# Kernel optimization log

Measured on AMD Instinct MI355X. Metric: run time of the kernel, lower is better.

Reference implementation:

```python
import jax, jax.numpy as jnp
import numpy as np

DIM = 512
HEADS = 8
DIM_HEAD = 64
INNER = HEADS * DIM_HEAD          # 512
CPB_DIM = DIM // 2                # 256 (ContinuousPositionBias hidden dim)
FF_INNER = int(DIM * 4 * 2 / 3)   # 1365 (GEGLU inner dim)
B, C, F, H, W = 2, 512, 8, 32, 32
SCALE = DIM_HEAD ** -0.5


def setup_inputs() -> dict:
    key = jax.random.key(0)
    ks = jax.random.split(key, 24)
    def rnd(k, shape, s=0.02):
        return jax.random.normal(k, shape, jnp.float32) * s
    return {
        "x": jax.random.normal(ks[0], (B, C, F, W, W), jnp.float32)[:, :, :, :H, :],
        # spatial attention
        "sa_gamma": jnp.ones((DIM,), jnp.float32),
        "sa_wq": rnd(ks[1], (DIM, INNER)),
        "sa_wkv": rnd(ks[2], (DIM, 2 * INNER)),
        "sa_wo": rnd(ks[3], (INNER, DIM)),
        # temporal attention
        "ta_gamma": jnp.ones((DIM,), jnp.float32),
        "ta_wq": rnd(ks[4], (DIM, INNER)),
        "ta_wkv": rnd(ks[5], (DIM, 2 * INNER)),
        "ta_wo": rnd(ks[6], (INNER, DIM)),
        # spatial ContinuousPositionBias MLP (num_dims=2, layers=2)
        "sp_w1": rnd(ks[7], (2, CPB_DIM), 0.1), "sp_b1": jnp.zeros((CPB_DIM,), jnp.float32),
        "sp_w2": rnd(ks[8], (CPB_DIM, CPB_DIM), 0.05), "sp_b2": jnp.zeros((CPB_DIM,), jnp.float32),
        "sp_w3": rnd(ks[9], (CPB_DIM, HEADS), 0.05), "sp_b3": jnp.zeros((HEADS,), jnp.float32),
        # temporal ContinuousPositionBias MLP (num_dims=1)
        "tp_w1": rnd(ks[10], (1, CPB_DIM), 0.1), "tp_b1": jnp.zeros((CPB_DIM,), jnp.float32),
        "tp_w2": rnd(ks[11], (CPB_DIM, CPB_DIM), 0.05), "tp_b2": jnp.zeros((CPB_DIM,), jnp.float32),
        "tp_w3": rnd(ks[12], (CPB_DIM, HEADS), 0.05), "tp_b3": jnp.zeros((HEADS,), jnp.float32),
        # FeedForward: Conv3d 1x1 (no bias) -> GEGLU -> RMSNorm -> Conv3d 1x1
        "ff_win": rnd(ks[13], (DIM, 2 * FF_INNER)),
        "ff_gamma": jnp.ones((FF_INNER,), jnp.float32),
        "ff_wout": rnd(ks[14], (FF_INNER, DIM)),
    }


def _rms_last(x, g):
    # torch: F.normalize(x, dim=-1) * sqrt(C) * gamma
    nrm = jnp.sqrt(jnp.sum(x * x, axis=-1, keepdims=True))
    return x / jnp.maximum(nrm, 1e-12) * jnp.sqrt(jnp.float32(x.shape[-1])) * g


def _mlp_bias(rel, w1, b1, w2, b2, w3, b3):
    h = jax.nn.silu(rel @ w1 + b1)
    h = jax.nn.silu(h @ w2 + b2)
    return h @ w3 + b3  # [R, heads]


def _cpb_2d(h, w, params):
    ry = jnp.arange(-(h - 1), h, dtype=jnp.float32)
    rx = jnp.arange(-(w - 1), w, dtype=jnp.float32)
    gy, gx = jnp.meshgrid(ry, rx, indexing='ij')
    rel = jnp.stack([gy, gx], -1).reshape(-1, 2)          # [(2h-1)(2w-1), 2]
    tab = _mlp_bias(rel, *params)                          # [R, heads]
    py, px = jnp.meshgrid(jnp.arange(h), jnp.arange(w), indexing='ij')
    pos = jnp.stack([py.reshape(-1), px.reshape(-1)], -1)  # [n, 2]
    d = pos[:, None, :] - pos[None, :, :]                  # [n, n, 2]
    idx = (d[..., 0] + h - 1) * (2 * w - 1) + (d[..., 1] + w - 1)
    return jnp.transpose(tab[idx], (2, 0, 1))              # [heads, n, n]


def _cpb_1d(f, params):
    rel = jnp.arange(-(f - 1), f, dtype=jnp.float32)[:, None]
    tab = _mlp_bias(rel, *params)                          # [2f-1, heads]
    p = jnp.arange(f)
    idx = p[:, None] - p[None, :] + f - 1
    return jnp.transpose(tab[idx], (2, 0, 1))              # [heads, f, f]


def _attn(x, gamma, wq, wkv, wo, bias):
    # x: [b, n, c]; manual softmax(QK^T*scale + bias)V (flash disabled by pos_bias)
    xn = _rms_last(x, gamma)
    q = xn @ wq
    k, v = jnp.split(xn @ wkv, 2, axis=-1)
    b, n, _ = q.shape
    rs = lambda t: t.reshape(b, n, HEADS, DIM_HEAD).transpose(0, 2, 1, 3)
    q, k, v = rs(q), rs(k), rs(v)
    s = jnp.einsum('bhid,bhjd->bhij', q, k) * SCALE + bias[None]
    a = jax.nn.softmax(s, axis=-1)
    o = jnp.einsum('bhij,bhjd->bhid', a, v)
    o = o.transpose(0, 2, 1, 3).reshape(b, n, INNER)
    return o @ wo


def _ff(x, win, gamma, wout):
    # x: [b, f, h, w, c] channel-last; Conv3d 1x1 == channel einsum
    hdn = jnp.einsum('bfhwc,co->bfhwo', x, win)
    a, gate = jnp.split(hdn, 2, axis=-1)
    y = a * jax.nn.gelu(gate, approximate=False)           # GEGLU (torch exact gelu)
    # shift_token: chunk channels, shift second half by +1 frame
    c1 = (FF_INNER + 1) // 2
    t1, t2 = y[..., :c1], y[..., c1:]
    t2 = jnp.pad(t2, ((0, 0), (1, 0), (0, 0), (0, 0), (0, 0)))[:, :-1]
    y = jnp.concatenate([t1, t2], axis=-1)
    yn = _rms_last(y, gamma)                               # RMSNorm over channels
    return jnp.einsum('bfhwi,ic->bfhwc', yn, wout)


def reference(x, sa_gamma, sa_wq, sa_wkv, sa_wo, ta_gamma, ta_wq, ta_wkv, ta_wo,
              sp_w1, sp_b1, sp_w2, sp_b2, sp_w3, sp_b3,
              tp_w1, tp_b1, tp_w2, tp_b2, tp_w3, tp_b3,
              ff_win, ff_gamma, ff_wout):
    b, c, f, h, w = x.shape
    xl = jnp.transpose(x, (0, 2, 3, 4, 1))                 # b f h w c
    # spatial attention over (h w) tokens, batched over (b f)
    xs = xl.reshape(b * f, h * w, c)
    sp_bias = _cpb_2d(h, w, (sp_w1, sp_b1, sp_w2, sp_b2, sp_w3, sp_b3))
    xs = _attn(xs, sa_gamma, sa_wq, sa_wkv, sa_wo, sp_bias) + xs
    xv = xs.reshape(b, f, h, w, c)
    # temporal attention over f tokens, batched over (b h w)
    xt = jnp.transpose(xv, (0, 2, 3, 1, 4)).reshape(b * h * w, f, c)
    tp_bias = _cpb_1d(f, (tp_w1, tp_b1, tp_w2, tp_b2, tp_w3, tp_b3))
    xt = _attn(xt, ta_gamma, ta_wq, ta_wkv, ta_wo, tp_bias) + xt
    xv = jnp.transpose(xt.reshape(b, h, w, f, c), (0, 3, 1, 2, 4))
    # GEGLU feedforward with token shift
    xv = _ff(xv, ff_win, ff_gamma, ff_wout) + xv
    return jnp.transpose(xv, (0, 4, 1, 2, 3))              # b c f h w
```

## Files before the change

kernel.cpp:

```cpp
#include <hip/hip_runtime.h>
#include <cstdint>
#include <cstddef>

typedef __bf16 bf16_t;
typedef __bf16 bf16x8 __attribute__((ext_vector_type(8)));
typedef __bf16 bf16x4 __attribute__((ext_vector_type(4)));
typedef float floatx4 __attribute__((ext_vector_type(4)));

__device__ __forceinline__ float wred_sum(float v) {
#pragma unroll
  for (int off = 32; off > 0; off >>= 1) v += __shfl_xor(v, off);
  return v;
}
__device__ __forceinline__ void async16(const void* g, void* l) {
  __builtin_amdgcn_global_load_lds((const __attribute__((address_space(1))) void*)g,
                                   (__attribute__((address_space(3))) void*)l, 16, 0, 0);
}

template <int MODE>
__global__ __launch_bounds__(256) void st_gemm(
    const bf16_t* __restrict__ A, const bf16_t* __restrict__ B, void* Cp, void* Cp2,
    const float* Res, int M, int N, int K, int lda, int ldb, int ldc, int nb1,
    long long sa1, long long sa2, long long sb1, long long sb2,
    long long sc1, long long sc2) {
  __shared__ bf16_t sA[128 * 32];
  __shared__ bf16_t sB[128 * 32];
  const int z = blockIdx.z;
  const int z1 = z % nb1, z2 = z / nb1;
  A += z1 * sa1 + z2 * sa2;
  B += z1 * sb1 + z2 * sb2;
  const long long coff = z1 * sc1 + z2 * sc2;
  const int tid = threadIdx.x;
  const int bm = blockIdx.x, bn = blockIdx.y;
  const int lane = tid & 63;
  const int wave = tid >> 6;
  const int wm = (wave >> 1) * 64, wn = (wave & 1) * 64;
  const int rowf = lane & 15, qc = lane >> 4;
  const int fco = (qc ^ ((rowf >> 1) & 3)) * 8;

  const bf16_t* aSrc[2];
  const bf16_t* bSrc[2];
  char* aDst[2];
  char* bDst[2];
#pragma unroll
  for (int it = 0; it < 2; ++it) {
    int slot = it * 256 + tid;
    int mi = slot >> 2, kc = slot & 3;
    int cs = kc ^ ((mi >> 1) & 3);
    int ar = bm * 128 + mi; if (ar > M - 1) ar = M - 1;
    int br = bn * 128 + mi; if (br > N - 1) br = N - 1;
    aSrc[it] = A + (size_t)ar * lda + cs * 8;
    bSrc[it] = B + (size_t)br * ldb + cs * 8;
    aDst[it] = (char*)sA + slot * 16;
    bDst[it] = (char*)sB + slot * 16;
  }

  floatx4 acc[4][4];
#pragma unroll
  for (int i = 0; i < 4; ++i)
#pragma unroll
    for (int j = 0; j < 4; ++j) acc[i][j] = floatx4{0.f, 0.f, 0.f, 0.f};

  for (int kt = 0; kt < K; kt += 32) {
#pragma unroll
    for (int it = 0; it < 2; ++it) {
      async16(aSrc[it] + kt, aDst[it]);
      async16(bSrc[it] + kt, bDst[it]);
    }
    __syncthreads();
    bf16x8 af[4], bv[4];
#pragma unroll
    for (int i = 0; i < 4; ++i) {
      af[i] = *(const bf16x8*)(sA + (wm + i * 16 + rowf) * 32 + fco);
      bv[i] = *(const bf16x8*)(sB + (wn + i * 16 + rowf) * 32 + fco);
    }
#pragma unroll
    for (int i = 0; i < 4; ++i)
#pragma unroll
      for (int j = 0; j < 4; ++j)
        acc[i][j] = __builtin_amdgcn_mfma_f32_16x16x32_bf16(af[i], bv[j], acc[i][j], 0, 0, 0);
    __syncthreads();
  }

  const int cl = lane & 15;
  const int rowBase = bm * 128 + wm + (lane >> 4) * 4;
  if (MODE == 5) {
    bf16_t* yb = (bf16_t*)Cp;
    const int cg0 = ((bn * 128 + wn) >> 5) * 16;
#pragma unroll
    for (int i = 0; i < 4; ++i) {
#pragma unroll
      for (int p = 0; p < 2; ++p) {
        int c = cg0 + p * 16 + cl;
        if (c >= 1365) continue;
#pragma unroll
        for (int r = 0; r < 4; ++r) {
          int row = rowBase + i * 16 + r;
          if (row >= M) continue;
          float a = acc[i][2 * p][r];
          float gt = acc[i][2 * p + 1][r];
          float zz = gt * (0.7978845608f + 0.03567740814f * gt * gt);
          float u = __builtin_exp2f(-2.8853900817779268f * zz);
          float y = a * gt / (1.f + u);
          yb[(size_t)row * ldc + c] = (bf16_t)y;
        }
      }
    }
    return;
  }
  const int colBase = bn * 128 + wn + cl;
#pragma unroll
  for (int i = 0; i < 4; ++i) {
#pragma unroll
    for (int j = 0; j < 4; ++j) {
      int col = colBase + j * 16;
      if (col >= N) continue;
#pragma unroll
      for (int r = 0; r < 4; ++r) {
        int row = rowBase + i * 16 + r;
        if (row >= M) continue;
        long long inidx = coff + (long long)row * ldc + col;
        float v = acc[i][j][r];
        if (MODE >= 2) v += Res[inidx];
        if (MODE == 0) { ((float*)Cp)[inidx] = v; }
        else if (MODE == 1) { ((bf16_t*)Cp)[inidx] = (bf16_t)v; }
        else if (MODE == 2) { ((float*)Cp)[inidx] = v; }
        else if (MODE == 3) {
          int orow = (row & ~8191) | ((row & 1023) << 3) | ((row >> 10) & 7);
          ((float*)Cp)[coff + (long long)orow * ldc + col] = v;
        } else if (MODE == 4) {
          int orow = (row & ~8191) | ((row & 7) << 10) | ((row >> 3) & 1023);
          long long oidx = coff + (long long)orow * ldc + col;
          ((float*)Cp)[oidx] = v;
          ((bf16_t*)Cp2)[oidx] = (bf16_t)v;
        }
      }
    }
  }
}

__global__ __launch_bounds__(256) void st_transpose2d(
    const float* __restrict__ in, float* __restrict__ out, int R, int Cc,
    long long inb, long long outb) {
  __shared__ float tile[32][33];
  const int ct = blockIdx.x, rt = blockIdx.y, b = blockIdx.z;
  in += (long long)b * inb;
  out += (long long)b * outb;
  const int tx = threadIdx.x & 31, ty = threadIdx.x >> 5;
#pragma unroll
  for (int k = 0; k < 4; ++k) {
    int r = rt * 32 + ty + k * 8;
    int c = ct * 32 + tx;
    tile[ty + k * 8][tx] = in[(size_t)r * Cc + c];
  }
  __syncthreads();
#pragma unroll
  for (int k = 0; k < 4; ++k) {
    int c = ct * 32 + ty + k * 8;
    int r = rt * 32 + tx;
    out[(size_t)c * R + r] = tile[tx][ty + k * 8];
  }
}

__global__ void st_wtrans(const float* __restrict__ src, bf16_t* __restrict__ dst,
                          int K, int Kpad, int N, int srcld, int coloff, long total) {
  long idx = (long)blockIdx.x * 256 + threadIdx.x;
  if (idx >= total) return;
  int kp = (int)(idx % Kpad);
  int n = (int)(idx / Kpad);
  float v = (kp < K) ? src[(size_t)kp * srcld + coloff + n] : 0.f;
  dst[idx] = (bf16_t)v;
}

__global__ void st_wtrans_geglu(const float* __restrict__ src, bf16_t* __restrict__ dst,
                                long total) {
  long idx = (long)blockIdx.x * 256 + threadIdx.x;
  if (idx >= total) return;
  int kp = (int)(idx & 511);
  int n = (int)(idx >> 9);
  int c = ((n >> 5) << 4) + (n & 15);
  float v = 0.f;
  if (c < 1365) {
    int srccol = c + (((n >> 4) & 1) ? 1365 : 0);
    v = src[(size_t)kp * 2730 + srccol];
  }
  dst[idx] = (bf16_t)v;
}

__global__ __launch_bounds__(256) void st_cpb(
    const float* __restrict__ w1, const float* __restrict__ b1,
    const float* __restrict__ w2, const float* __restrict__ b2,
    const float* __restrict__ w3, const float* __restrict__ b3,
    float* __restrict__ tab2d, float* __restrict__ tab1d, int two_d) {
  const int pos = blockIdx.x, t = threadIdx.x;
  float r0, r1 = 0.f;
  if (two_d) { r0 = (float)(pos / 63 - 31); r1 = (float)(pos % 63 - 31); }
  else { r0 = (float)(pos - 7); }
  __shared__ float sh[256];
  float h = r0 * w1[t] + (two_d ? r1 * w1[256 + t] : 0.f) + b1[t];
  h = h / (1.f + expf(-h));
  sh[t] = h;
  __syncthreads();
  float h2 = b2[t];
  for (int j = 0; j < 256; ++j) h2 += sh[j] * w2[j * 256 + t];
  h2 = h2 / (1.f + expf(-h2));
  __syncthreads();
  sh[t] = h2;
  __syncthreads();
  if (t < 8) {
    float o = b3[t];
    for (int j = 0; j < 256; ++j) o += sh[j] * w3[j * 8 + t];
    if (two_d) tab2d[t * 4000 + pos] = o * 8.0f;
    else tab1d[t * 15 + pos] = o;
  }
}

__global__ __launch_bounds__(256) void st_rmsnorm(const float* __restrict__ x,
                                                  const float* __restrict__ gamma,
                                                  bf16_t* __restrict__ y) {
  const int token = blockIdx.x * 4 + (threadIdx.x >> 6);
  const int lane = threadIdx.x & 63;
  const float* xr = x + (size_t)token * 512;
  float v[8];
  float ss = 0.f;
#pragma unroll
  for (int k = 0; k < 8; ++k) { v[k] = xr[k * 64 + lane]; ss += v[k] * v[k]; }
  ss = wred_sum(ss);
  const float r = 22.627416998f / fmaxf(sqrtf(ss), 1e-12f);
  bf16_t* yr = y + (size_t)token * 512;
#pragma unroll
  for (int k = 0; k < 8; ++k) yr[k * 64 + lane] = (bf16_t)(v[k] * r * gamma[k * 64 + lane]);
}

__global__ __launch_bounds__(256) void st_vtrans(const bf16_t* __restrict__ qkv,
                                                 bf16_t* __restrict__ vT) {
  __shared__ float tile[32][33];
  const int jt = blockIdx.x, dt = blockIdx.y, z = blockIdx.z;
  const int bf = z >> 3, h = z & 7;
  const int tx = threadIdx.x & 31, ty = threadIdx.x >> 5;
#pragma unroll
  for (int k = 0; k < 4; ++k) {
    int j = jt * 32 + ty + k * 8;
    int d = dt * 32 + tx;
    tile[ty + k * 8][tx] = (float)qkv[((size_t)(bf * 1024 + j)) * 1536 + 1024 + h * 64 + d];
  }
  __syncthreads();
#pragma unroll
  for (int k = 0; k < 4; ++k) {
    int d = dt * 32 + ty + k * 8;
    int j = jt * 32 + tx;
    vT[((size_t)z * 64 + d) * 1024 + j] = (bf16_t)tile[tx][ty + k * 8];
  }
}

__global__ __launch_bounds__(256, 4) void st_flash(
    const bf16_t* __restrict__ qkv, const bf16_t* __restrict__ vT,
    const float* __restrict__ tab2f, bf16_t* __restrict__ ob) {
  __shared__ __align__(16) bf16_t ldsK[2][32 * 64];
  __shared__ __align__(16) bf16_t ldsV[2][64 * 32];
  __shared__ __align__(16) bf16_t ldsP[4 * 32 * 32];
  __shared__ __align__(16) float ldsT[2208];
  const int qtile = blockIdx.x;
  const int z = blockIdx.y;
  const int bf = z >> 3, h = z & 7;
  const int tid = threadIdx.x;
  const int lane = tid & 63, wave = tid >> 6;
  const int cl = lane & 15, g = lane >> 4;
  const size_t qkvBase = (size_t)bf * 1024 * 1536 + h * 64;
  const int eoff = (qtile * 252) & ~3;
  const bf16_t* Kp = qkv + qkvBase + 512;
  const bf16_t* Vp = vT + (size_t)z * 65536;

#pragma unroll
  for (int it = 0; it < 3; ++it) {
    int s = it * 256 + tid;
    if (s < 552) async16(tab2f + h * 4000 + eoff + s * 4, (char*)ldsT + s * 16);
  }
  {
    int row = tid >> 3, c = tid & 7, cs = c ^ (row & 7);
    async16(Kp + (size_t)row * 1536 + cs * 8, (char*)ldsK[0] + tid * 16);
    int rv = tid >> 2, cv = tid & 3, csv = cv ^ (rv & 3);
    async16(Vp + (size_t)rv * 1024 + csv * 8, (char*)ldsV[0] + tid * 16);
  }
  bf16x8 aq[2][2];
#pragma unroll
  for (int it = 0; it < 2; ++it)
#pragma unroll
    for (int ks = 0; ks < 2; ++ks) {
      int row = qtile * 128 + wave * 32 + it * 16 + cl;
      aq[it][ks] = *(const bf16x8*)(qkv + qkvBase + (size_t)row * 1536 + (ks * 4 + g) * 8);
    }
  __syncthreads();

  int fiB[2];
#pragma unroll
  for (int it = 0; it < 2; ++it) {
    int i = qtile * 128 + wave * 32 + it * 16 + cl;
    fiB[it] = (i >> 5) * 63 + (i & 31) + 1984 - eoff;
  }
  float lsum[2] = {0.f, 0.f};
  floatx4 oacc[4][2];
#pragma unroll
  for (int dt = 0; dt < 4; ++dt)
#pragma unroll
    for (int it = 0; it < 2; ++it) oacc[dt][it] = floatx4{0.f, 0.f, 0.f, 0.f};

  bf16_t* ldsPw = ldsP + wave * (32 * 32);
  const float SC = 0.18033688011112042f;

#pragma unroll 2
  for (int t = 0; t < 32; ++t) {
    const int p = t & 1;
    if (t < 31) {
      const int j1 = (t + 1) * 32;
      int row = tid >> 3, c = tid & 7, cs = c ^ (row & 7);
      async16(Kp + (size_t)(j1 + row) * 1536 + cs * 8, (char*)ldsK[p ^ 1] + tid * 16);
      int rv = tid >> 2, cv = tid & 3, csv = cv ^ (rv & 3);
      async16(Vp + (size_t)rv * 1024 + j1 + csv * 8, (char*)ldsV[p ^ 1] + tid * 16);
    }
    const int j0 = t * 32;
#pragma unroll
    for (int jt = 0; jt < 2; ++jt) {
      int jb = j0 + jt * 16 + g * 4;
      int fjb = (jb >> 5) * 63 + (jb & 31);
      floatx4 sj[2];
#pragma unroll
      for (int it = 0; it < 2; ++it) {
        int idx0 = fiB[it] - fjb;
        sj[it] = floatx4{ldsT[idx0], ldsT[idx0 - 1], ldsT[idx0 - 2], ldsT[idx0 - 3]};
      }
#pragma unroll
      for (int ks = 0; ks < 2; ++ks) {
        int row = jt * 16 + cl;
        bf16x8 kf = *(const bf16x8*)(ldsK[p] + row * 64 + (((ks * 4 + g) ^ (row & 7))) * 8);
#pragma unroll
        for (int it = 0; it < 2; ++it)
          sj[it] = __builtin_amdgcn_mfma_f32_16x16x32_bf16(kf, aq[it][ks], sj[it], 0, 0, 0);
      }
      int gg = jt * 2 + (g >> 1);
#pragma unroll
      for (int it = 0; it < 2; ++it) {
        float e0 = __builtin_exp2f(sj[it][0] * SC);
        float e1 = __builtin_exp2f(sj[it][1] * SC);
        float e2 = __builtin_exp2f(sj[it][2] * SC);
        float e3 = __builtin_exp2f(sj[it][3] * SC);
        lsum[it] += (e0 + e1) + (e2 + e3);
        bf16x4 pv = {(bf16_t)e0, (bf16_t)e1, (bf16_t)e2, (bf16_t)e3};
        *(bf16x4*)((char*)ldsPw + (it * 16 + cl) * 64 +
                   ((gg ^ (cl & 3)) * 16 + (g & 1) * 8)) = pv;
      }
    }
    {
      bf16x8 pB[2];
#pragma unroll
      for (int it = 0; it < 2; ++it)
        pB[it] = *(const bf16x8*)((char*)ldsPw + (it * 16 + cl) * 64 + ((g ^ (cl & 3)) * 16));
#pragma unroll
      for (int dt = 0; dt < 4; ++dt) {
        int row = dt * 16 + cl;
        bf16x8 vf = *(const bf16x8*)(ldsV[p] + row * 32 + ((g ^ (row & 3)) * 8));
#pragma unroll
        for (int it = 0; it < 2; ++it)
          oacc[dt][it] = __builtin_amdgcn_mfma_f32_16x16x32_bf16(vf, pB[it], oacc[dt][it], 0, 0, 0);
      }
    }
    __syncthreads();
  }
  float inv[2];
#pragma unroll
  for (int it = 0; it < 2; ++it) {
    float s = lsum[it];
    s += __shfl_xor(s, 16);
    s += __shfl_xor(s, 32);
    inv[it] = 1.f / s;
  }
#pragma unroll
  for (int it = 0; it < 2; ++it) {
    int i = qtile * 128 + wave * 32 + it * 16 + cl;
    size_t base = ((size_t)bf * 1024 + i) * 512 + h * 64 + g * 4;
#pragma unroll
    for (int dt = 0; dt < 4; ++dt) {
      bf16x4 ov = {(bf16_t)(oacc[dt][it][0] * inv[it]), (bf16_t)(oacc[dt][it][1] * inv[it]),
                   (bf16_t)(oacc[dt][it][2] * inv[it]), (bf16_t)(oacc[dt][it][3] * inv[it])};
      *(bf16x4*)(ob + base + dt * 16) = ov;
    }
  }
}

__global__ __launch_bounds__(256) void st_tattn2(const bf16_t* __restrict__ qkv,
                                                 const float* __restrict__ tabf,
                                                 bf16_t* __restrict__ o) {
  const int wg = blockIdx.x * 4 + (threadIdx.x >> 6);
  const int bhw = wg >> 3, head = wg & 7;
  const int lane = threadIdx.x & 63;
  const size_t base = (size_t)bhw * 8 * 1536 + head * 64 + lane;
  float q[8], k[8], v[8];
#pragma unroll
  for (int f = 0; f < 8; ++f) {
    q[f] = (float)qkv[base + (size_t)f * 1536];
    k[f] = (float)qkv[base + (size_t)f * 1536 + 512];
    v[f] = (float)qkv[base + (size_t)f * 1536 + 1024];
  }
  float p[64];
#pragma unroll
  for (int i = 0; i < 8; ++i)
#pragma unroll
    for (int j = 0; j < 8; ++j) p[i * 8 + j] = q[i] * k[j];
#pragma unroll
  for (int st = 32; st >= 1; st >>= 1) {
    const bool hi = (lane & st) != 0;
#pragma unroll
    for (int m = 0; m < st; ++m) {
      float give = hi ? p[m] : p[m + st];
      float keep = hi ? p[m + st] : p[m];
      p[m] = keep + __shfl_xor(give, st);
    }
  }
  const int i = lane >> 3, j = lane & 7;
  float e = __expf(p[0] * 0.125f + tabf[head * 15 + i - j + 7]);
  float sm = e;
  sm += __shfl_xor(sm, 1);
  sm += __shfl_xor(sm, 2);
  sm += __shfl_xor(sm, 4);
  const float prob = e / sm;
  float acc[8];
#pragma unroll
  for (int ii = 0; ii < 8; ++ii) acc[ii] = 0.f;
#pragma unroll
  for (int ii = 0; ii < 8; ++ii)
#pragma unroll
    for (int jj = 0; jj < 8; ++jj)
      acc[ii] += __shfl(prob, ii * 8 + jj) * v[jj];
#pragma unroll
  for (int ii = 0; ii < 8; ++ii)
    o[(size_t)(bhw * 8 + ii) * 512 + head * 64 + lane] = (bf16_t)acc[ii];
}

__global__ __launch_bounds__(256) void st_glu(const bf16_t* __restrict__ y,
                                              const float* __restrict__ gamma,
                                              bf16_t* __restrict__ yn) {
  const int t = blockIdx.x;
  const int tid = threadIdx.x;
  const int f = (t >> 10) & 7;
  float yv[6];
  float ss = 0.f;
#pragma unroll
  for (int kk = 0; kk < 6; ++kk) {
    int c = kk * 256 + tid;
    float v = 0.f;
    if (c < 1365) {
      long src = t;
      bool valid = true;
      if (c >= 683) { if (f == 0) valid = false; else src = t - 1024; }
      if (valid) v = (float)y[src * 1365 + c];
    }
    yv[kk] = v;
    ss += v * v;
  }
  __shared__ float red[4];
  ss = wred_sum(ss);
  if ((tid & 63) == 0) red[tid >> 6] = ss;
  __syncthreads();
  ss = red[0] + red[1] + red[2] + red[3];
  const float r = sqrtf(1365.f) / fmaxf(sqrtf(ss), 1e-12f);
#pragma unroll
  for (int kk = 0; kk < 6; ++kk) {
    int c = kk * 256 + tid;
    if (c < 1365) yn[(size_t)t * 1376 + c] = (bf16_t)(yv[kk] * r * gamma[c]);
  }
  if (tid < 11) yn[(size_t)t * 1376 + 1365 + tid] = (bf16_t)0.f;
}

extern "C" void kernel_launch(void* const* d_in, const int* in_sizes, int n_in,
                              void* d_out, int out_size, void* d_ws, size_t ws_size,
                              hipStream_t stream) {
  const float* x        = (const float*)d_in[0];
  const float* sa_gamma = (const float*)d_in[1];
  const float* sa_wq    = (const float*)d_in[2];
  const float* sa_wkv   = (const float*)d_in[3];
  const float* sa_wo    = (const float*)d_in[4];
  const float* ta_gamma = (const float*)d_in[5];
  const float* ta_wq    = (const float*)d_in[6];
  const float* ta_wkv   = (const float*)d_in[7];
  const float* ta_wo    = (const float*)d_in[8];
  const float* sp_w1 = (const float*)d_in[9];
  const float* sp_b1 = (const float*)d_in[10];
  const float* sp_w2 = (const float*)d_in[11];
  const float* sp_b2 = (const float*)d_in[12];
  const float* sp_w3 = (const float*)d_in[13];
  const float* sp_b3 = (const float*)d_in[14];
  const float* tp_w1 = (const float*)d_in[15];
  const float* tp_b1 = (const float*)d_in[16];
  const float* tp_w2 = (const float*)d_in[17];
  const float* tp_b2 = (const float*)d_in[18];
  const float* tp_w3 = (const float*)d_in[19];
  const float* tp_b3 = (const float*)d_in[20];
  const float* ff_win   = (const float*)d_in[21];
  const float* ff_gamma = (const float*)d_in[22];
  const float* ff_wout  = (const float*)d_in[23];
  float* outp = (float*)d_out;

  char* ws = (char*)d_ws;
  size_t off = 0;
  auto alloc = [&](size_t bytes) -> char* {
    char* p = ws + off;
    off += (bytes + 255) & ~(size_t)255;
    return p;
  };
  const long T = 16384;
  float*  xs  = (float*)alloc((size_t)T * 512 * 4);
  bf16_t* xn  = (bf16_t*)alloc((size_t)T * 512 * 2);
  char*   R2  = alloc((size_t)T * 1536 * 2);
  char*   R3  = alloc((size_t)T * 1536 * 2);
  char*   R4  = alloc((size_t)T * 1376 * 2);
  bf16_t* wqkvT_sa = (bf16_t*)alloc(1536ULL * 512 * 2);
  bf16_t* woT_sa   = (bf16_t*)alloc(512ULL * 512 * 2);
  bf16_t* wqkvT_ta = (bf16_t*)alloc(1536ULL * 512 * 2);
  bf16_t* woT_ta   = (bf16_t*)alloc(512ULL * 512 * 2);
  bf16_t* winT  = (bf16_t*)alloc(2752ULL * 512 * 2);
  bf16_t* woutT = (bf16_t*)alloc(512ULL * 1376 * 2);
  float*  tab2f = (float*)alloc(8 * 4000 * 4);
  float*  tabf  = (float*)alloc(8 * 15 * 4);

  bf16_t* qkv  = (bf16_t*)R2;
  bf16_t* ybuf = (bf16_t*)R2;
  bf16_t* vT   = (bf16_t*)R3;
  float*  xt   = (float*)R3;
  bf16_t* ob_s = xn;
  bf16_t* ob_t = (bf16_t*)R4;
  bf16_t* ynb  = (bf16_t*)R4;

  st_transpose2d<<<dim3(256, 16, 2), 256, 0, stream>>>(x, xs, 512, 8192,
                                                       (long long)512 * 8192, (long long)512 * 8192);
  auto wt = [&](const float* src, bf16_t* dst, int K, int Kpad, int N, int srcld, int coloff) {
    long tot = (long)N * Kpad;
    st_wtrans<<<dim3((tot + 255) / 256), 256, 0, stream>>>(src, dst, K, Kpad, N, srcld, coloff, tot);
  };
  wt(sa_wq, wqkvT_sa, 512, 512, 512, 512, 0);
  wt(sa_wkv, wqkvT_sa + 512 * 512, 512, 512, 1024, 1024, 0);
  wt(sa_wo, woT_sa, 512, 512, 512, 512, 0);
  wt(ta_wq, wqkvT_ta, 512, 512, 512, 512, 0);
  wt(ta_wkv, wqkvT_ta + 512 * 512, 512, 512, 1024, 1024, 0);
  wt(ta_wo, woT_ta, 512, 512, 512, 512, 0);
  st_wtrans_geglu<<<dim3((2752 * 512) / 256), 256, 0, stream>>>(ff_win, winT, 2752L * 512);
  wt(ff_wout, woutT, 1365, 1376, 512, 512, 0);
  st_cpb<<<dim3(3969), 256, 0, stream>>>(sp_w1, sp_b1, sp_w2, sp_b2, sp_w3, sp_b3, tab2f, tabf, 1);
  st_cpb<<<dim3(15), 256, 0, stream>>>(tp_w1, tp_b1, tp_w2, tp_b2, tp_w3, tp_b3, tab2f, tabf, 0);

  st_rmsnorm<<<dim3(4096), 256, 0, stream>>>(xs, sa_gamma, xn);
  st_gemm<1><<<dim3(128, 12, 1), 256, 0, stream>>>(
      xn, wqkvT_sa, (void*)qkv, nullptr, nullptr, 16384, 1536, 512, 512, 512, 1536, 1, 0, 0, 0, 0, 0, 0);
  st_vtrans<<<dim3(32, 2, 128), 256, 0, stream>>>(qkv, vT);
  st_flash<<<dim3(8, 128), 256, 0, stream>>>(qkv, vT, tab2f, ob_s);
  st_gemm<3><<<dim3(128, 4, 1), 256, 0, stream>>>(
      ob_s, woT_sa, (void*)xt, nullptr, xs, 16384, 512, 512, 512, 512, 512, 1, 0, 0, 0, 0, 0, 0);

  st_rmsnorm<<<dim3(4096), 256, 0, stream>>>(xt, ta_gamma, xn);
  st_gemm<1><<<dim3(128, 12, 1), 256, 0, stream>>>(
      xn, wqkvT_ta, (void*)qkv, nullptr, nullptr, 16384, 1536, 512, 512, 512, 1536, 1, 0, 0, 0, 0, 0, 0);
  st_tattn2<<<dim3(4096), 256, 0, stream>>>(qkv, tabf, ob_t);
  st_gemm<4><<<dim3(128, 4, 1), 256, 0, stream>>>(
      ob_t, woT_ta, (void*)xs, (void*)xn, xt, 16384, 512, 512, 512, 512, 512, 1, 0, 0, 0, 0, 0, 0);

  st_gemm<5><<<dim3(128, 22, 1), 256, 0, stream>>>(
      xn, winT, (void*)ybuf, nullptr, nullptr, 16384, 2752, 512, 512, 512, 1365, 1, 0, 0, 0, 0, 0, 0);
  st_glu<<<dim3(16384), 256, 0, stream>>>(ybuf, ff_gamma, ynb);
  st_gemm<2><<<dim3(128, 4, 1), 256, 0, stream>>>(
      ynb, woutT, (void*)xs, nullptr, xs, 16384, 512, 1376, 1376, 1376, 512, 1, 0, 0, 0, 0, 0, 0);

  st_transpose2d<<<dim3(16, 256, 2), 256, 0, stream>>>(xs, outp, 8192, 512,
                                                       (long long)8192 * 512, (long long)8192 * 512);
}
```

Baseline: 685.7 us.

## Add 256x256-tile triple-buffered GEMM for QKV and GEGLU projections

Adds a new 512-thread GEMM kernel with 256x256 output tiles, a three-stage async global-to-LDS buffer ring, split A/B prefetch interleaved with MFMA phases, s_setprio around the MFMA blocks, and a swizzled block order for L2 locality. It replaces the two QKV projections and the GEGLU input projection. The GEGLU weight is padded to 2816 columns so the N dimension divides the larger tile. The intent is more reuse per tile and hiding load latency behind compute. The cost is more LDS and registers per block and fewer blocks in flight. The old kernel's batching arguments and MODE 5 path are removed.

```diff
diff --git a/kernel.cpp b/kernel.cpp
--- a/kernel.cpp
+++ b/kernel.cpp
@@ -18,18 +18,152 @@
 }
 
 template <int MODE>
+__global__ __launch_bounds__(512, 2) void st_gemm8(
+    const bf16_t* __restrict__ A, const bf16_t* __restrict__ B, void* Cp,
+    int M, int N, int K, int lda, int ldb, int ldc) {
+  __shared__ bf16_t sA[3][256 * 32];
+  __shared__ bf16_t sB[3][256 * 32];
+  const int tid = threadIdx.x;
+  const int lane = tid & 63, wave = tid >> 6;
+  const int wr = wave >> 2, wc = wave & 3;
+  const int cl = lane & 15, cfc = lane >> 4;
+  const int gx = gridDim.x;
+  const int flat = blockIdx.y * gx + blockIdx.x;
+  const int qq = (gx * gridDim.y) >> 3;
+  const int swz = (flat & 7) * qq + (flat >> 3);
+  const int bm = swz % gx, bn = swz / gx;
+
+  const bf16_t* aSg[2];
+  const bf16_t* bSg[2];
+  int sOff[2];
+#pragma unroll
+  for (int i = 0; i < 2; ++i) {
+    int slot = i * 512 + tid;
+    int line = slot >> 3, w8 = slot & 7;
+    int nfc = w8 ^ (line & 7);
+    int row = line * 2 + (nfc >> 2), c = nfc & 3;
+    aSg[i] = A + (size_t)(bm * 256 + row) * lda + c * 8;
+    bSg[i] = B + (size_t)(bn * 256 + row) * ldb + c * 8;
+    sOff[i] = slot * 16;
+  }
+  const int fch = (((((cl & 1) << 2) | cfc) ^ (cl >> 1))) * 16;
+  const int aBase = wr * 8192 + (cl >> 1) * 128 + fch;
+  const int bBase = wc * 4096 + (cl >> 1) * 128 + fch;
+
+  floatx4 acc[8][4];
+#pragma unroll
+  for (int m = 0; m < 8; ++m)
+#pragma unroll
+    for (int n = 0; n < 4; ++n) acc[m][n] = floatx4{0.f, 0.f, 0.f, 0.f};
+
+  async16(aSg[0], (char*)sA[0] + sOff[0]);
+  async16(aSg[1], (char*)sA[0] + sOff[1]);
+  async16(bSg[0], (char*)sB[0] + sOff[0]);
+  async16(bSg[1], (char*)sB[0] + sOff[1]);
+  async16(aSg[0] + 32, (char*)sA[1] + sOff[0]);
+  async16(aSg[1] + 32, (char*)sA[1] + sOff[1]);
+  async16(bSg[0] + 32, (char*)sB[1] + sOff[0]);
+  async16(bSg[1] + 32, (char*)sB[1] + sOff[1]);
+  __builtin_amdgcn_sched_barrier(0);
+  asm volatile("s_waitcnt vmcnt(4)" ::: "memory");
+  __builtin_amdgcn_s_barrier();
+
+  const int NT = K >> 5;
+  int bcur = 0, bnx = 2;
+#pragma unroll 1
+  for (int t = 0; t < NT; ++t) {
+    const char* sAc = (const char*)sA[bcur];
+    const char* sBc = (const char*)sB[bcur];
+    char* sAn = (char*)sA[bnx];
+    char* sBn = (char*)sB[bnx];
+    const int kt2 = (t + 2) << 5;
+    const bool pf = (t + 2) < NT;
+    bf16x8 af[4], bv[4];
+    if (pf) {
+      async16(aSg[0] + kt2, sAn + sOff[0]);
+      async16(aSg[1] + kt2, sAn + sOff[1]);
+    }
+#pragma unroll
+    for (int m = 0; m < 4; ++m) af[m] = *(const bf16x8*)(sAc + aBase + m * 1024);
+#pragma unroll
+    for (int n = 0; n < 4; ++n) bv[n] = *(const bf16x8*)(sBc + bBase + n * 1024);
+    __builtin_amdgcn_sched_barrier(0);
+    __builtin_amdgcn_s_barrier();
+    __builtin_amdgcn_s_setprio(1);
+#pragma unroll
+    for (int m = 0; m < 4; ++m)
+#pragma unroll
+      for (int n = 0; n < 4; ++n)
+        acc[m][n] = __builtin_amdgcn_mfma_f32_16x16x32_bf16(af[m], bv[n], acc[m][n], 0, 0, 0);
+    __builtin_amdgcn_s_setprio(0);
+    __builtin_amdgcn_sched_barrier(0);
+    __builtin_amdgcn_s_barrier();
+    if (pf) {
+      async16(bSg[0] + kt2, sBn + sOff[0]);
+      async16(bSg[1] + kt2, sBn + sOff[1]);
+    }
+#pragma unroll
+    for (int m = 0; m < 4; ++m) af[m] = *(const bf16x8*)(sAc + aBase + (m + 4) * 1024);
+    __builtin_amdgcn_sched_barrier(0);
+    __builtin_amdgcn_s_barrier();
+    __builtin_amdgcn_s_setprio(1);
+#pragma unroll
+    for (int m = 0; m < 4; ++m)
+#pragma unroll
+      for (int n = 0; n < 4; ++n)
+        acc[m + 4][n] = __builtin_amdgcn_mfma_f32_16x16x32_bf16(af[m], bv[n], acc[m + 4][n], 0, 0, 0);
+    __builtin_amdgcn_s_setprio(0);
+    __builtin_amdgcn_sched_barrier(0);
+    if (t < NT - 1) {
+      if (t == NT - 2) asm volatile("s_waitcnt vmcnt(0)" ::: "memory");
+      else             asm volatile("s_waitcnt vmcnt(4)" ::: "memory");
+    }
+    __builtin_amdgcn_s_barrier();
+    bcur = (bcur == 2) ? 0 : bcur + 1;
+    bnx = (bnx == 2) ? 0 : bnx + 1;
+  }
+
+  const int rowB = bm * 256 + wr * 128 + cfc * 4;
+  if (MODE == 1) {
+    bf16_t* yb = (bf16_t*)Cp;
+    const int colB = bn * 256 + wc * 64 + cl;
+#pragma unroll
+    for (int m = 0; m < 8; ++m)
+#pragma unroll
+      for (int n = 0; n < 4; ++n) {
+        size_t base = (size_t)(rowB + m * 16) * ldc + colB + n * 16;
+#pragma unroll
+        for (int r = 0; r < 4; ++r) yb[base + (size_t)r * ldc] = (bf16_t)acc[m][n][r];
+      }
+  } else {
+    bf16_t* yb = (bf16_t*)Cp;
+    const int cg0 = ((bn * 256 + wc * 64) >> 5) * 16;
+#pragma unroll
+    for (int m = 0; m < 8; ++m)
+#pragma unroll
+      for (int p = 0; p < 2; ++p) {
+        int c = cg0 + p * 16 + cl;
+        if (c >= 1365) continue;
+#pragma unroll
+        for (int r = 0; r < 4; ++r) {
+          int row = rowB + m * 16 + r;
+          float a = acc[m][2 * p][r];
+          float gt = acc[m][2 * p + 1][r];
+          float zz = gt * (0.7978845608f + 0.03567740814f * gt * gt);
+          float u = __builtin_exp2f(-2.8853900817779268f * zz);
+          float y = a * gt / (1.f + u);
+          yb[(size_t)row * ldc + c] = (bf16_t)y;
+        }
+      }
+  }
+}
+
+template <int MODE>
 __global__ __launch_bounds__(256) void st_gemm(
     const bf16_t* __restrict__ A, const bf16_t* __restrict__ B, void* Cp, void* Cp2,
-    const float* Res, int M, int N, int K, int lda, int ldb, int ldc, int nb1,
-    long long sa1, long long sa2, long long sb1, long long sb2,
-    long long sc1, long long sc2) {
+    const float* Res, int M, int N, int K, int lda, int ldb, int ldc) {
   __shared__ bf16_t sA[128 * 32];
   __shared__ bf16_t sB[128 * 32];
-  const int z = blockIdx.z;
-  const int z1 = z % nb1, z2 = z / nb1;
-  A += z1 * sa1 + z2 * sa2;
-  B += z1 * sb1 + z2 * sb2;
-  const long long coff = z1 * sc1 + z2 * sc2;
   const int tid = threadIdx.x;
   const int bm = blockIdx.x, bn = blockIdx.y;
   const int lane = tid & 63;
@@ -84,30 +218,6 @@
 
   const int cl = lane & 15;
   const int rowBase = bm * 128 + wm + (lane >> 4) * 4;
-  if (MODE == 5) {
-    bf16_t* yb = (bf16_t*)Cp;
-    const int cg0 = ((bn * 128 + wn) >> 5) * 16;
-#pragma unroll
-    for (int i = 0; i < 4; ++i) {
-#pragma unroll
-      for (int p = 0; p < 2; ++p) {
-        int c = cg0 + p * 16 + cl;
-        if (c >= 1365) continue;
-#pragma unroll
-        for (int r = 0; r < 4; ++r) {
-          int row = rowBase + i * 16 + r;
-          if (row >= M) continue;
-          float a = acc[i][2 * p][r];
-          float gt = acc[i][2 * p + 1][r];
-          float zz = gt * (0.7978845608f + 0.03567740814f * gt * gt);
-          float u = __builtin_exp2f(-2.8853900817779268f * zz);
-          float y = a * gt / (1.f + u);
-          yb[(size_t)row * ldc + c] = (bf16_t)y;
-        }
-      }
-    }
-    return;
-  }
   const int colBase = bn * 128 + wn + cl;
 #pragma unroll
   for (int i = 0; i < 4; ++i) {
@@ -119,18 +229,15 @@
       for (int r = 0; r < 4; ++r) {
         int row = rowBase + i * 16 + r;
         if (row >= M) continue;
-        long long inidx = coff + (long long)row * ldc + col;
-        float v = acc[i][j][r];
-        if (MODE >= 2) v += Res[inidx];
-        if (MODE == 0) { ((float*)Cp)[inidx] = v; }
-        else if (MODE == 1) { ((bf16_t*)Cp)[inidx] = (bf16_t)v; }
-        else if (MODE == 2) { ((float*)Cp)[inidx] = v; }
+        long long inidx = (long long)row * ldc + col;
+        float v = acc[i][j][r] + Res[inidx];
+        if (MODE == 2) { ((float*)Cp)[inidx] = v; }
         else if (MODE == 3) {
           int orow = (row & ~8191) | ((row & 1023) << 3) | ((row >> 10) & 7);
-          ((float*)Cp)[coff + (long long)orow * ldc + col] = v;
+          ((float*)Cp)[(long long)orow * ldc + col] = v;
         } else if (MODE == 4) {
           int orow = (row & ~8191) | ((row & 7) << 10) | ((row >> 3) & 1023);
-          long long oidx = coff + (long long)orow * ldc + col;
+          long long oidx = (long long)orow * ldc + col;
           ((float*)Cp)[oidx] = v;
           ((bf16_t*)Cp2)[oidx] = (bf16_t)v;
         }
@@ -517,7 +624,7 @@
   bf16_t* woT_sa   = (bf16_t*)alloc(512ULL * 512 * 2);
   bf16_t* wqkvT_ta = (bf16_t*)alloc(1536ULL * 512 * 2);
   bf16_t* woT_ta   = (bf16_t*)alloc(512ULL * 512 * 2);
-  bf16_t* winT  = (bf16_t*)alloc(2752ULL * 512 * 2);
+  bf16_t* winT  = (bf16_t*)alloc(2816ULL * 512 * 2);
   bf16_t* woutT = (bf16_t*)alloc(512ULL * 1376 * 2);
   float*  tab2f = (float*)alloc(8 * 4000 * 4);
   float*  tabf  = (float*)alloc(8 * 15 * 4);
@@ -542,31 +649,31 @@
   wt(ta_wq, wqkvT_ta, 512, 512, 512, 512, 0);
   wt(ta_wkv, wqkvT_ta + 512 * 512, 512, 512, 1024, 1024, 0);
   wt(ta_wo, woT_ta, 512, 512, 512, 512, 0);
-  st_wtrans_geglu<<<dim3((2752 * 512) / 256), 256, 0, stream>>>(ff_win, winT, 2752L * 512);
+  st_wtrans_geglu<<<dim3((2816 * 512) / 256), 256, 0, stream>>>(ff_win, winT, 2816L * 512);
   wt(ff_wout, woutT, 1365, 1376, 512, 512, 0);
   st_cpb<<<dim3(3969), 256, 0, stream>>>(sp_w1, sp_b1, sp_w2, sp_b2, sp_w3, sp_b3, tab2f, tabf, 1);
   st_cpb<<<dim3(15), 256, 0, stream>>>(tp_w1, tp_b1, tp_w2, tp_b2, tp_w3, tp_b3, tab2f, tabf, 0);
 
   st_rmsnorm<<<dim3(4096), 256, 0, stream>>>(xs, sa_gamma, xn);
-  st_gemm<1><<<dim3(128, 12, 1), 256, 0, stream>>>(
-      xn, wqkvT_sa, (void*)qkv, nullptr, nullptr, 16384, 1536, 512, 512, 512, 1536, 1, 0, 0, 0, 0, 0, 0);
+  st_gemm8<1><<<dim3(64, 6), 512, 0, stream>>>(
+      xn, wqkvT_sa, (void*)qkv, 16384, 1536, 512, 512, 512, 1536);
   st_vtrans<<<dim3(32, 2, 128), 256, 0, stream>>>(qkv, vT);
   st_flash<<<dim3(8, 128), 256, 0, stream>>>(qkv, vT, tab2f, ob_s);
   st_gemm<3><<<dim3(128, 4, 1), 256, 0, stream>>>(
-      ob_s, woT_sa, (void*)xt, nullptr, xs, 16384, 512, 512, 512, 512, 512, 1, 0, 0, 0, 0, 0, 0);
+      ob_s, woT_sa, (void*)xt, nullptr, xs, 16384, 512, 512, 512, 512, 512);
 
   st_rmsnorm<<<dim3(4096), 256, 0, stream>>>(xt, ta_gamma, xn);
-  st_gemm<1><<<dim3(128, 12, 1), 256, 0, stream>>>(
-      xn, wqkvT_ta, (void*)qkv, nullptr, nullptr, 16384, 1536, 512, 512, 512, 1536, 1, 0, 0, 0, 0, 0, 0);
+  st_gemm8<1><<<dim3(64, 6), 512, 0, stream>>>(
+      xn, wqkvT_ta, (void*)qkv, 16384, 1536, 512, 512, 512, 1536);
   st_tattn2<<<dim3(4096), 256, 0, stream>>>(qkv, tabf, ob_t);
   st_gemm<4><<<dim3(128, 4, 1), 256, 0, stream>>>(
-      ob_t, woT_ta, (void*)xs, (void*)xn, xt, 16384, 512, 512, 512, 512, 512, 1, 0, 0, 0, 0, 0, 0);
-
-  st_gemm<5><<<dim3(128, 22, 1), 256, 0, stream>>>(
-      xn, winT, (void*)ybuf, nullptr, nullptr, 16384, 2752, 512, 512, 512, 1365, 1, 0, 0, 0, 0, 0, 0);
+      ob_t, woT_ta, (void*)xs, (void*)xn, xt, 16384, 512, 512, 512, 512, 512);
+
+  st_gemm8<5><<<dim3(64, 11), 512, 0, stream>>>(
+      xn, winT, (void*)ybuf, 16384, 2816, 512, 512, 512, 1365);
   st_glu<<<dim3(16384), 256, 0, stream>>>(ybuf, ff_gamma, ynb);
   st_gemm<2><<<dim3(128, 4, 1), 256, 0, stream>>>(
-      ynb, woutT, (void*)xs, nullptr, xs, 16384, 512, 1376, 1376, 1376, 512, 1, 0, 0, 0, 0, 0, 0);
+      ynb, woutT, (void*)xs, nullptr, xs, 16384, 512, 1376, 1376, 1376, 512);
 
   st_transpose2d<<<dim3(16, 256, 2), 256, 0, stream>>>(xs, outp, 8192, 512,
                                                        (long long)8192 * 512, (long long)8192 * 512);
```

Result: slower. 740.4 us (+8.0%).

## Triple-buffer GEMM LDS tiles with async prefetch two k-steps ahead

Applied to the files above, without the earlier changes.

The GEMM main loop now uses three LDS buffers per operand and issues global-to-LDS async loads for tile t+2 while computing tile t. Explicit vmcnt waits plus a single s_barrier per iteration replace the two __syncthreads per k-step, so global load latency overlaps with MFMA work. Unused batched-stride parameters and MODE 0 are removed. LDS use triples to 48KB per block, which may lower occupancy, and correctness depends on the hand-written waitcnt counts.

```diff
diff --git a/kernel.cpp b/kernel.cpp
--- a/kernel.cpp
+++ b/kernel.cpp
@@ -20,16 +20,9 @@
 template <int MODE>
 __global__ __launch_bounds__(256) void st_gemm(
     const bf16_t* __restrict__ A, const bf16_t* __restrict__ B, void* Cp, void* Cp2,
-    const float* Res, int M, int N, int K, int lda, int ldb, int ldc, int nb1,
-    long long sa1, long long sa2, long long sb1, long long sb2,
-    long long sc1, long long sc2) {
-  __shared__ bf16_t sA[128 * 32];
-  __shared__ bf16_t sB[128 * 32];
-  const int z = blockIdx.z;
-  const int z1 = z % nb1, z2 = z / nb1;
-  A += z1 * sa1 + z2 * sa2;
-  B += z1 * sb1 + z2 * sb2;
-  const long long coff = z1 * sc1 + z2 * sc2;
+    const float* Res, int M, int N, int K, int lda, int ldb, int ldc) {
+  __shared__ bf16_t sA[3][128 * 32];
+  __shared__ bf16_t sB[3][128 * 32];
   const int tid = threadIdx.x;
   const int bm = blockIdx.x, bn = blockIdx.y;
   const int lane = tid & 63;
@@ -40,8 +33,7 @@
 
   const bf16_t* aSrc[2];
   const bf16_t* bSrc[2];
-  char* aDst[2];
-  char* bDst[2];
+  int sOff[2];
 #pragma unroll
   for (int it = 0; it < 2; ++it) {
     int slot = it * 256 + tid;
@@ -51,8 +43,7 @@
     int br = bn * 128 + mi; if (br > N - 1) br = N - 1;
     aSrc[it] = A + (size_t)ar * lda + cs * 8;
     bSrc[it] = B + (size_t)br * ldb + cs * 8;
-    aDst[it] = (char*)sA + slot * 16;
-    bDst[it] = (char*)sB + slot * 16;
+    sOff[it] = slot * 16;
   }
 
   floatx4 acc[4][4];
@@ -61,25 +52,55 @@
 #pragma unroll
     for (int j = 0; j < 4; ++j) acc[i][j] = floatx4{0.f, 0.f, 0.f, 0.f};
 
-  for (int kt = 0; kt < K; kt += 32) {
-#pragma unroll
-    for (int it = 0; it < 2; ++it) {
-      async16(aSrc[it] + kt, aDst[it]);
-      async16(bSrc[it] + kt, bDst[it]);
-    }
-    __syncthreads();
+  const int NT = K >> 5;
+#pragma unroll
+  for (int it = 0; it < 2; ++it) {
+    async16(aSrc[it], (char*)sA[0] + sOff[it]);
+    async16(bSrc[it], (char*)sB[0] + sOff[it]);
+  }
+#pragma unroll
+  for (int it = 0; it < 2; ++it) {
+    async16(aSrc[it] + 32, (char*)sA[1] + sOff[it]);
+    async16(bSrc[it] + 32, (char*)sB[1] + sOff[it]);
+  }
+  __builtin_amdgcn_sched_barrier(0);
+  asm volatile("s_waitcnt vmcnt(4)" ::: "memory");
+  __builtin_amdgcn_s_barrier();
+  __builtin_amdgcn_sched_barrier(0);
+
+  int bcur = 0, bnx = 2;
+#pragma unroll 1
+  for (int t = 0; t < NT; ++t) {
+    const bf16_t* sAc = sA[bcur];
+    const bf16_t* sBc = sB[bcur];
     bf16x8 af[4], bv[4];
 #pragma unroll
     for (int i = 0; i < 4; ++i) {
-      af[i] = *(const bf16x8*)(sA + (wm + i * 16 + rowf) * 32 + fco);
-      bv[i] = *(const bf16x8*)(sB + (wn + i * 16 + rowf) * 32 + fco);
+      af[i] = *(const bf16x8*)(sAc + (wm + i * 16 + rowf) * 32 + fco);
+      bv[i] = *(const bf16x8*)(sBc + (wn + i * 16 + rowf) * 32 + fco);
+    }
+    if (t + 2 < NT) {
+      const int kt2 = (t + 2) * 32;
+#pragma unroll
+      for (int it = 0; it < 2; ++it) {
+        async16(aSrc[it] + kt2, (char*)sA[bnx] + sOff[it]);
+        async16(bSrc[it] + kt2, (char*)sB[bnx] + sOff[it]);
+      }
     }
 #pragma unroll
     for (int i = 0; i < 4; ++i)
 #pragma unroll
       for (int j = 0; j < 4; ++j)
         acc[i][j] = __builtin_amdgcn_mfma_f32_16x16x32_bf16(af[i], bv[j], acc[i][j], 0, 0, 0);
-    __syncthreads();
+    if (t + 1 < NT) {
+      __builtin_amdgcn_sched_barrier(0);
+      if (t + 2 < NT) asm volatile("s_waitcnt vmcnt(4)" ::: "memory");
+      else            asm volatile("s_waitcnt vmcnt(0)" ::: "memory");
+      __builtin_amdgcn_s_barrier();
+      __builtin_amdgcn_sched_barrier(0);
+    }
+    bcur = (bcur == 2) ? 0 : bcur + 1;
+    bnx = (bnx == 2) ? 0 : bnx + 1;
   }
 
   const int cl = lane & 15;
@@ -119,18 +140,17 @@
       for (int r = 0; r < 4; ++r) {
         int row = rowBase + i * 16 + r;
         if (row >= M) continue;
-        long long inidx = coff + (long long)row * ldc + col;
+        long long inidx = (long long)row * ldc + col;
         float v = acc[i][j][r];
         if (MODE >= 2) v += Res[inidx];
-        if (MODE == 0) { ((float*)Cp)[inidx] = v; }
-        else if (MODE == 1) { ((bf16_t*)Cp)[inidx] = (bf16_t)v; }
+        if (MODE == 1) { ((bf16_t*)Cp)[inidx] = (bf16_t)v; }
         else if (MODE == 2) { ((float*)Cp)[inidx] = v; }
         else if (MODE == 3) {
           int orow = (row & ~8191) | ((row & 1023) << 3) | ((row >> 10) & 7);
-          ((float*)Cp)[coff + (long long)orow * ldc + col] = v;
+          ((float*)Cp)[(long long)orow * ldc + col] = v;
         } else if (MODE == 4) {
           int orow = (row & ~8191) | ((row & 7) << 10) | ((row >> 3) & 1023);
-          long long oidx = coff + (long long)orow * ldc + col;
+          long long oidx = (long long)orow * ldc + col;
           ((float*)Cp)[oidx] = v;
           ((bf16_t*)Cp2)[oidx] = (bf16_t)v;
         }
@@ -548,25 +568,25 @@
   st_cpb<<<dim3(15), 256, 0, stream>>>(tp_w1, tp_b1, tp_w2, tp_b2, tp_w3, tp_b3, tab2f, tabf, 0);
 
   st_rmsnorm<<<dim3(4096), 256, 0, stream>>>(xs, sa_gamma, xn);
-  st_gemm<1><<<dim3(128, 12, 1), 256, 0, stream>>>(
-      xn, wqkvT_sa, (void*)qkv, nullptr, nullptr, 16384, 1536, 512, 512, 512, 1536, 1, 0, 0, 0, 0, 0, 0);
+  st_gemm<1><<<dim3(128, 12), 256, 0, stream>>>(
+      xn, wqkvT_sa, (void*)qkv, nullptr, nullptr, 16384, 1536, 512, 512, 512, 1536);
   st_vtrans<<<dim3(32, 2, 128), 256, 0, stream>>>(qkv, vT);
   st_flash<<<dim3(8, 128), 256, 0, stream>>>(qkv, vT, tab2f, ob_s);
-  st_gemm<3><<<dim3(128, 4, 1), 256, 0, stream>>>(
-      ob_s, woT_sa, (void*)xt, nullptr, xs, 16384, 512, 512, 512, 512, 512, 1, 0, 0, 0, 0, 0, 0);
+  st_gemm<3><<<dim3(128, 4), 256, 0, stream>>>(
+      ob_s, woT_sa, (void*)xt, nullptr, xs, 16384, 512, 512, 512, 512, 512);
 
   st_rmsnorm<<<dim3(4096), 256, 0, stream>>>(xt, ta_gamma, xn);
-  st_gemm<1><<<dim3(128, 12, 1), 256, 0, stream>>>(
-      xn, wqkvT_ta, (void*)qkv, nullptr, nullptr, 16384, 1536, 512, 512, 512, 1536, 1, 0, 0, 0, 0, 0, 0);
+  st_gemm<1><<<dim3(128, 12), 256, 0, stream>>>(
+      xn, wqkvT_ta, (void*)qkv, nullptr, nullptr, 16384, 1536, 512, 512, 512, 1536);
   st_tattn2<<<dim3(4096), 256, 0, stream>>>(qkv, tabf, ob_t);
-  st_gemm<4><<<dim3(128, 4, 1), 256, 0, stream>>>(
-      ob_t, woT_ta, (void*)xs, (void*)xn, xt, 16384, 512, 512, 512, 512, 512, 1, 0, 0, 0, 0, 0, 0);
-
-  st_gemm<5><<<dim3(128, 22, 1), 256, 0, stream>>>(
-      xn, winT, (void*)ybuf, nullptr, nullptr, 16384, 2752, 512, 512, 512, 1365, 1, 0, 0, 0, 0, 0, 0);
+  st_gemm<4><<<dim3(128, 4), 256, 0, stream>>>(
+      ob_t, woT_ta, (void*)xs, (void*)xn, xt, 16384, 512, 512, 512, 512, 512);
+
+  st_gemm<5><<<dim3(128, 22), 256, 0, stream>>>(
+      xn, winT, (void*)ybuf, nullptr, nullptr, 16384, 2752, 512, 512, 512, 1365);
   st_glu<<<dim3(16384), 256, 0, stream>>>(ybuf, ff_gamma, ynb);
-  st_gemm<2><<<dim3(128, 4, 1), 256, 0, stream>>>(
-      ynb, woutT, (void*)xs, nullptr, xs, 16384, 512, 1376, 1376, 1376, 512, 1, 0, 0, 0, 0, 0, 0);
+  st_gemm<2><<<dim3(128, 4), 256, 0, stream>>>(
+      ynb, woutT, (void*)xs, nullptr, xs, 16384, 512, 1376, 1376, 1376, 512);
 
   st_transpose2d<<<dim3(16, 256, 2), 256, 0, stream>>>(xs, outp, 8192, 512,
                                                        (long long)8192 * 512, (long long)8192 * 512);
```

Measured after the change: 654.9 us. 1.05x faster.
